# Performance work log

Measured on AMD Instinct MI355X. Metric: run time of the kernel, lower is better.

## Reference

```python
import jax, jax.numpy as jnp
import numpy as np

N = 50000
E = 600000
IN_CH = 128
HID = 256
OUT_CH = 64
R = 8


def setup_inputs() -> dict:
    key = jax.random.key(0)
    ks = jax.random.split(key, 12)
    x = jax.random.normal(ks[0], (N, IN_CH), dtype=jnp.float32)
    edge_index = jax.random.randint(ks[1], (2, E), 0, N, dtype=jnp.int32)
    edge_type = jax.random.randint(ks[2], (E,), 0, R, dtype=jnp.int32)
    s1 = 1.0 / np.sqrt(IN_CH)
    s2 = 1.0 / np.sqrt(HID)
    W1 = jax.random.uniform(ks[3], (R, IN_CH, HID), jnp.float32, -s1, s1)
    root1 = jax.random.uniform(ks[4], (IN_CH, HID), jnp.float32, -s1, s1)
    b1 = jnp.zeros((HID,), jnp.float32)
    W2 = jax.random.uniform(ks[5], (R, HID, HID), jnp.float32, -s2, s2)
    root2 = jax.random.uniform(ks[6], (HID, HID), jnp.float32, -s2, s2)
    b2 = jnp.zeros((HID,), jnp.float32)
    lin_W = jax.random.uniform(ks[7], (HID, OUT_CH), jnp.float32, -s2, s2)
    lin_b = jnp.zeros((OUT_CH,), jnp.float32)
    return {
        "x": x, "edge_index": edge_index, "edge_type": edge_type,
        "W1": W1, "root1": root1, "b1": b1,
        "W2": W2, "root2": root2, "b2": b2,
        "lin_W": lin_W, "lin_b": lin_b,
    }


def rgcn_conv(x, src, dst, edge_type, W, root, b):
    # out_i = root x_i + b + sum_r mean_{j in N_r(i)} W_r x_j  (PyG RGCNConv, aggr='mean')
    num_rel = W.shape[0]
    n = x.shape[0]
    out = x @ root + b
    x_src = x[src]  # [E, d_in] gathered once, masked per relation
    for r in range(num_rel):
        mask = (edge_type == r)
        msg = jnp.where(mask[:, None], x_src, 0.0)
        agg = jax.ops.segment_sum(msg, dst, num_segments=n)          # [N, d_in]
        cnt = jax.ops.segment_sum(mask.astype(x.dtype), dst, num_segments=n)
        agg = agg / jnp.maximum(cnt, 1.0)[:, None]                    # mean per relation
        out = out + agg @ W[r]
    return out


def reference(x, edge_index, edge_type, W1, root1, b1, W2, root2, b2, lin_W, lin_b):
    src, dst = edge_index[0], edge_index[1]
    h = jax.nn.relu(rgcn_conv(x, src, dst, edge_type, W1, root1, b1))
    h = jax.nn.relu(rgcn_conv(h, src, dst, edge_type, W2, root2, b2))
    logits = h @ lin_W + lin_b
    return jax.nn.log_softmax(logits, axis=-1)
```

## Files before the change

### kernel.cpp

```cpp
#include <hip/hip_runtime.h>
#include <hip/hip_bf16.h>

#define N_NODES 50000
#define E_EDGES 600000
#define IN_CH 128
#define HID 256
#define OUT_CH 64
#define NREL 8
#define HALF1 25000

typedef __attribute__((ext_vector_type(8))) short bf16x8;
typedef __attribute__((ext_vector_type(4))) float f32x4;

__device__ __forceinline__ float bf2f(unsigned short u) {
    union { unsigned int i; float f; } x; x.i = ((unsigned int)u) << 16; return x.f;
}
__device__ __forceinline__ unsigned short f2bf(float f) {
    __hip_bfloat16 b = __float2bfloat16(f);
    return *reinterpret_cast<unsigned short*>(&b);
}
__device__ __forceinline__ void gload_lds16(const void* g, void* l) {
    __builtin_amdgcn_global_load_lds(
        (const __attribute__((address_space(1))) unsigned int*)g,
        (__attribute__((address_space(3))) unsigned int*)l, 16, 0, 0);
}

__global__ void k_deg(const int* __restrict__ dst, int* __restrict__ deg) {
    int e = blockIdx.x * blockDim.x + threadIdx.x;
    if (e < E_EDGES) atomicAdd(&deg[dst[e]], 1);
}

__global__ __launch_bounds__(256) void k_scanA(const int* __restrict__ deg,
                                               int* __restrict__ offs,
                                               int* __restrict__ bsum) {
    __shared__ int wexcl[4];
    const int tid = threadIdx.x;
    const int lane = tid & 63;
    const int wid = tid >> 6;
    const int i = blockIdx.x * 256 + tid;
    const int v = (i < N_NODES) ? deg[i] : 0;
    int incl = v;
#pragma unroll
    for (int s = 1; s < 64; s <<= 1) {
        int t = __shfl_up(incl, s);
        if (lane >= s) incl += t;
    }
    __shared__ int wsum[4];
    if (lane == 63) wsum[wid] = incl;
    __syncthreads();
    if (tid == 0) {
        int run = 0;
#pragma unroll
        for (int w = 0; w < 4; w++) { wexcl[w] = run; run += wsum[w]; }
        bsum[blockIdx.x] = run;
    }
    __syncthreads();
    if (i < N_NODES) offs[i] = wexcl[wid] + incl - v;
}

__global__ __launch_bounds__(256) void k_scanB(int* __restrict__ bsum, int nb) {
    __shared__ int wexcl[4];
    __shared__ int wsum[4];
    const int tid = threadIdx.x;
    const int lane = tid & 63;
    const int wid = tid >> 6;
    const int v = (tid < nb) ? bsum[tid] : 0;
    int incl = v;
#pragma unroll
    for (int s = 1; s < 64; s <<= 1) {
        int t = __shfl_up(incl, s);
        if (lane >= s) incl += t;
    }
    if (lane == 63) wsum[wid] = incl;
    __syncthreads();
    if (tid == 0) {
        int run = 0;
#pragma unroll
        for (int w = 0; w < 4; w++) { wexcl[w] = run; run += wsum[w]; }
    }
    __syncthreads();
    if (tid < nb) bsum[tid] = wexcl[wid] + incl - v;
}

__global__ __launch_bounds__(256) void k_scanC(int* __restrict__ offs,
                                               const int* __restrict__ bsum) {
    const int i = blockIdx.x * 256 + threadIdx.x;
    if (i < N_NODES) offs[i] += bsum[blockIdx.x];
    if (i == 0) offs[N_NODES] = E_EDGES;
}

__global__ void k_place(const int* __restrict__ src, const int* __restrict__ dst,
                        const int* __restrict__ etype, const int* __restrict__ offs,
                        int* __restrict__ cursor, int* __restrict__ ekey) {
    int e = blockIdx.x * blockDim.x + threadIdx.x;
    if (e < E_EDGES) {
        int d = dst[e];
        int p = atomicAdd(&cursor[d], 1);
        ekey[offs[d] + p] = (etype[e] << 16) | src[e];
    }
}

__global__ __launch_bounds__(256) void k_wsort(const int* __restrict__ offs,
                                               int* __restrict__ ekey,
                                               int* __restrict__ relOffs) {
    const int w = threadIdx.x >> 6;
    const int t = threadIdx.x & 63;
    const int i = blockIdx.x * 4 + w;
    if (i >= N_NODES) return;
    const int lo = offs[i], hi = offs[i + 1];
    const int deg = hi - lo;
    if (deg == 0) {
        if (t < 9) relOffs[i * 9 + t] = lo;
        return;
    }
    if (deg <= 64) {
        const int key = (t < deg) ? ekey[lo + t] : 0x7FFFFFFF;
        int rank = 0;
#pragma unroll
        for (int s = 0; s < 64; s++) {
            const int ok = __shfl(key, s);
            rank += (int)((ok < key) | ((ok == key) & (s < t)));
        }
        if (t < deg) ekey[lo + rank] = key;
        const int rel = key >> 16;
        if (t == 0) relOffs[i * 9] = lo;
        int run = lo;
#pragma unroll
        for (int r = 0; r < NREL; r++) {
            unsigned long long b = __ballot((t < deg) && (rel == r));
            run += (int)__popcll(b);
            if (t == 0) relOffs[i * 9 + r + 1] = run;
        }
    } else if (t == 0) {
        for (int a = lo + 1; a < hi; a++) {
            int k = ekey[a];
            int b = a - 1;
            while (b >= lo && ekey[b] > k) { ekey[b + 1] = ekey[b]; b--; }
            ekey[b + 1] = k;
        }
        int p = lo;
        relOffs[i * 9] = lo;
#pragma unroll
        for (int r = 0; r < NREL; r++) {
            while (p < hi && (ekey[p] >> 16) == r) p++;
            relOffs[i * 9 + r + 1] = p;
        }
    }
}

#define PREP_CVT 6250
#define PREP_WT1 1152
#define PREP_WT2 2304
#define PREP_WT3 128
__global__ __launch_bounds__(256) void k_prep(const float* __restrict__ x,
                                              unsigned short* __restrict__ xb,
                                              const float* __restrict__ root1,
                                              const float* __restrict__ W1,
                                              unsigned short* __restrict__ Wt1,
                                              const float* __restrict__ root2,
                                              const float* __restrict__ W2,
                                              unsigned short* __restrict__ Wt2,
                                              const float* __restrict__ linW,
                                              unsigned short* __restrict__ linWt) {
    const int b = blockIdx.x;
    if (b < PREP_CVT) {
        int i = b * 256 + threadIdx.x;
        float4 v = *(const float4*)&x[i * 4];
        short4 o;
        o.x = (short)f2bf(v.x); o.y = (short)f2bf(v.y);
        o.z = (short)f2bf(v.z); o.w = (short)f2bf(v.w);
        *(short4*)&xb[i * 4] = o;
    } else if (b < PREP_CVT + PREP_WT1) {
        int idx = (b - PREP_CVT) * 256 + threadIdx.x;
        int c = idx / 1152, k = idx % 1152;
        float v = (k < IN_CH) ? root1[k * 256 + c] : W1[(size_t)(k - IN_CH) * 256 + c];
        Wt1[idx] = f2bf(v);
    } else if (b < PREP_CVT + PREP_WT1 + PREP_WT2) {
        int idx = (b - PREP_CVT - PREP_WT1) * 256 + threadIdx.x;
        int c = idx / 2304, k = idx % 2304;
        float v = (k < HID) ? root2[k * 256 + c] : W2[(size_t)(k - HID) * 256 + c];
        Wt2[idx] = f2bf(v);
    } else {
        int idx = (b - PREP_CVT - PREP_WT1 - PREP_WT2) * 256 + threadIdx.x;
        int rp = idx / 256, k = idx % 256;
        int c = rp & 63;
        float w = linW[k * OUT_CH + c];
        unsigned short hi = f2bf(w);
        linWt[idx] = (rp < 64) ? hi : f2bf(w - bf2f(hi));
    }
}

template <int CH>
__global__ __launch_bounds__(256) void k_agg8(const unsigned short* __restrict__ xin,
                                              const int* __restrict__ relOffs,
                                              const int* __restrict__ ekey,
                                              unsigned short* __restrict__ agg,
                                              int base, int count) {
    const int w = threadIdx.x >> 6;
    const int t = threadIdx.x & 63;
    const int rel_node = blockIdx.x * 4 + w;
    if (rel_node >= count) return;
    const int node = base + rel_node;
    constexpr int VPT = CH / 64;
    const unsigned short* xcol = xin + t * VPT;
    unsigned short* orow = agg + (size_t)rel_node * (NREL * CH) + t * VPT;
    const int* ro = relOffs + node * 9;
    const int lo = ro[0];
    const int deg = ro[8] - lo;

    if (deg == 0) {
#pragma unroll
        for (int r = 0; r < NREL; r++) {
            if (VPT == 4) *(short4*)(orow + r * CH) = make_short4(0, 0, 0, 0);
            else *(short2*)(orow + r * CH) = make_short2(0, 0);
        }
        return;
    }

    if (deg <= 64) {
        const int kv = ekey[lo + ((t < deg) ? t : 0)];
#pragma unroll
        for (int r = 0; r < NREL; r++) {
            const int s = ro[r] - lo, e = ro[r + 1] - lo;
            const int len = e - s;
            float a0 = 0.f, a1 = 0.f, a2 = 0.f, a3 = 0.f;
            int j = s;
            for (; j + 2 <= e; j += 2) {
                const int k0 = __shfl(kv, j) & 0xFFFF;
                const int k1 = __shfl(kv, j + 1) & 0xFFFF;
                if (VPT == 4) {
                    short4 v0 = *(const short4*)(xcol + (size_t)k0 * CH);
                    short4 v1 = *(const short4*)(xcol + (size_t)k1 * CH);
                    a0 += bf2f((unsigned short)v0.x);
                    a1 += bf2f((unsigned short)v0.y);
                    a2 += bf2f((unsigned short)v0.z);
                    a3 += bf2f((unsigned short)v0.w);
                    a0 += bf2f((unsigned short)v1.x);
                    a1 += bf2f((unsigned short)v1.y);
                    a2 += bf2f((unsigned short)v1.z);
                    a3 += bf2f((unsigned short)v1.w);
                } else {
                    short2 v0 = *(const short2*)(xcol + (size_t)k0 * CH);
                    short2 v1 = *(const short2*)(xcol + (size_t)k1 * CH);
                    a0 += bf2f((unsigned short)v0.x);
                    a1 += bf2f((unsigned short)v0.y);
                    a0 += bf2f((unsigned short)v1.x);
                    a1 += bf2f((unsigned short)v1.y);
                }
            }
            if (j < e) {
                const int k0 = __shfl(kv, j) & 0xFFFF;
                if (VPT == 4) {
                    short4 v0 = *(const short4*)(xcol + (size_t)k0 * CH);
                    a0 += bf2f((unsigned short)v0.x);
                    a1 += bf2f((unsigned short)v0.y);
                    a2 += bf2f((unsigned short)v0.z);
                    a3 += bf2f((unsigned short)v0.w);
                } else {
                    short2 v0 = *(const short2*)(xcol + (size_t)k0 * CH);
                    a0 += bf2f((unsigned short)v0.x);
                    a1 += bf2f((unsigned short)v0.y);
                }
            }
            const float inv = (len > 0) ? 1.0f / (float)len : 0.0f;
            if (VPT == 4) {
                short4 o;
                o.x = (short)f2bf(a0 * inv);
                o.y = (short)f2bf(a1 * inv);
                o.z = (short)f2bf(a2 * inv);
                o.w = (short)f2bf(a3 * inv);
                *(short4*)(orow + r * CH) = o;
            } else {
                short2 o;
                o.x = (short)f2bf(a0 * inv);
                o.y = (short)f2bf(a1 * inv);
                *(short2*)(orow + r * CH) = o;
            }
        }
    } else {
#pragma unroll
        for (int r = 0; r < NREL; r++) {
            const int s = ro[r], e = ro[r + 1];
            float a0 = 0.f, a1 = 0.f, a2 = 0.f, a3 = 0.f;
            for (int ee = s; ee < e; ee++) {
                const int k = ekey[ee] & 0xFFFF;
                if (VPT == 4) {
                    short4 v = *(const short4*)(xcol + (size_t)k * CH);
                    a0 += bf2f((unsigned short)v.x);
                    a1 += bf2f((unsigned short)v.y);
                    a2 += bf2f((unsigned short)v.z);
                    a3 += bf2f((unsigned short)v.w);
                } else {
                    short2 v = *(const short2*)(xcol + (size_t)k * CH);
                    a0 += bf2f((unsigned short)v.x);
                    a1 += bf2f((unsigned short)v.y);
                }
            }
            const float inv = (e > s) ? 1.0f / (float)(e - s) : 0.0f;
            if (VPT == 4) {
                short4 o;
                o.x = (short)f2bf(a0 * inv);
                o.y = (short)f2bf(a1 * inv);
                o.z = (short)f2bf(a2 * inv);
                o.w = (short)f2bf(a3 * inv);
                *(short4*)(orow + r * CH) = o;
            } else {
                short2 o;
                o.x = (short)f2bf(a0 * inv);
                o.y = (short)f2bf(a1 * inv);
                *(short2*)(orow + r * CH) = o;
            }
        }
    }
}

__global__ __launch_bounds__(256) void k_mgemm(
    const unsigned short* __restrict__ Aroot, int rootK, int ldroot,
    const unsigned short* __restrict__ Aagg, int ldagg,
    const unsigned short* __restrict__ Wt, int ldWt, int Ktot,
    const float* __restrict__ bias, unsigned short* __restrict__ hbOut, int M,
    int rowsPerXcd) {
    __shared__ __align__(16) unsigned short Al[2][128 * 64];
    __shared__ __align__(16) unsigned short Bl[2][128 * 64];
    const int p = blockIdx.x;
    const int xcd = p & 7;
    const int col = (p >> 3) & 1;
    const int rIdx = p >> 4;
    const int row = xcd * rowsPerXcd + rIdx;
    if (row * 128 >= M) return;
    const int bm = row * 128;
    const int bn = col * 128;
    const int tid = threadIdx.x;
    const int wv = tid >> 6, ln = tid & 63;
    const int wr = (wv & 1) * 64;
    const int wc = (wv >> 1) * 64;
    const int lg = ln >> 4;
    const int lr = ln & 15;

    f32x4 acc[4][4];
#pragma unroll
    for (int m = 0; m < 4; m++)
#pragma unroll
        for (int n = 0; n < 4; n++) acc[m][n] = (f32x4){0.f, 0.f, 0.f, 0.f};

    int baseR[4], baseG[4], baseB[4];
#pragma unroll
    for (int q = 0; q < 4; q++) {
        int t = (wv * 4 + q) * 64 + ln;
        int r = t >> 3, ps = t & 7;
        int slog = ps ^ (r & 7);
        int rg = bm + r; if (rg > M - 1) rg = M - 1;
        baseR[q] = (rootK > 0) ? (rg * ldroot + slog * 8) : 0;
        baseG[q] = rg * ldagg + slog * 8 - rootK;
        baseB[q] = (bn + r) * ldWt + slog * 8;
    }

    auto stage = [&](int k0, int buf) {
        const bool inRoot = (k0 < rootK);
#pragma unroll
        for (int q = 0; q < 4; q++) {
            const unsigned short* sa =
                inRoot ? (Aroot + baseR[q] + k0) : (Aagg + baseG[q] + k0);
            gload_lds16(sa, &Al[buf][(wv * 4 + q) * 512]);
        }
#pragma unroll
        for (int q = 0; q < 4; q++) {
            gload_lds16(Wt + baseB[q] + k0, &Bl[buf][(wv * 4 + q) * 512]);
        }
    };

    const int nt = Ktot >> 6;
    stage(0, 0);
    asm volatile("s_waitcnt vmcnt(0)" ::: "memory");
    __syncthreads();

    int cur = 0;
    for (int t = 0; t < nt; ++t) {
        if (t + 1 < nt) stage((t + 1) << 6, cur ^ 1);
        __builtin_amdgcn_s_setprio(1);
#pragma unroll
        for (int kk = 0; kk < 2; kk++) {
            bf16x8 af[4], bfr[4];
#pragma unroll
            for (int m = 0; m < 4; m++) {
                int r = wr + 16 * m + lr;
                int ph = (kk * 4 + lg) ^ (r & 7);
                af[m] = *(const bf16x8*)&Al[cur][r * 64 + ph * 8];
            }
#pragma unroll
            for (int n = 0; n < 4; n++) {
                int c = wc + 16 * n + lr;
                int ph = (kk * 4 + lg) ^ (c & 7);
                bfr[n] = *(const bf16x8*)&Bl[cur][c * 64 + ph * 8];
            }
#pragma unroll
            for (int m = 0; m < 4; m++)
#pragma unroll
                for (int n = 0; n < 4; n++)
                    acc[m][n] = __builtin_amdgcn_mfma_f32_16x16x32_bf16(
                        af[m], bfr[n], acc[m][n], 0, 0, 0);
        }
        __builtin_amdgcn_s_setprio(0);
        if (t + 1 < nt) {
            asm volatile("s_waitcnt vmcnt(0)" ::: "memory");
            __syncthreads();
            cur ^= 1;
        }
    }

#pragma unroll
    for (int m = 0; m < 4; m++) {
#pragma unroll
        for (int reg = 0; reg < 4; reg++) {
            int r = bm + wr + 16 * m + lg * 4 + reg;
            if (r >= M) continue;
#pragma unroll
            for (int n = 0; n < 4; n++) {
                int c = bn + wc + 16 * n + lr;
                float v = acc[m][n][reg] + bias[c];
                hbOut[(size_t)r * 256 + c] = f2bf(fmaxf(v, 0.f));
            }
        }
    }
}

__global__ __launch_bounds__(256) void k_final3(const unsigned short* __restrict__ h,
                                                const unsigned short* __restrict__ linWt,
                                                const float* __restrict__ bias,
                                                float* __restrict__ out, int M) {
    __shared__ __align__(16) unsigned short Al[128 * 64];
    __shared__ __align__(16) unsigned short Bl[128 * 64];
    const int bm = blockIdx.x * 128;
    const int tid = threadIdx.x;
    const int wv = tid >> 6, ln = tid & 63;
    const int wr = wv * 32;
    const int lg = ln >> 4;
    const int lr = ln & 15;

    f32x4 acc[2][8];
#pragma unroll
    for (int m = 0; m < 2; m++)
#pragma unroll
        for (int n = 0; n < 8; n++) acc[m][n] = (f32x4){0.f, 0.f, 0.f, 0.f};

    int baseA[4], baseB[4];
#pragma unroll
    for (int q = 0; q < 4; q++) {
        int t = (wv * 4 + q) * 64 + ln;
        int r = t >> 3, ps = t & 7;
        int slog = ps ^ (r & 7);
        int rg = bm + r; if (rg > M - 1) rg = M - 1;
        baseA[q] = rg * HID + slog * 8;
        baseB[q] = r * HID + slog * 8;
    }

    for (int t = 0; t < 4; ++t) {
        if (t > 0) __syncthreads();
        const int k0 = t << 6;
#pragma unroll
        for (int q = 0; q < 4; q++)
            gload_lds16(h + baseA[q] + k0, &Al[(wv * 4 + q) * 512]);
#pragma unroll
        for (int q = 0; q < 4; q++)
            gload_lds16(linWt + baseB[q] + k0, &Bl[(wv * 4 + q) * 512]);
        asm volatile("s_waitcnt vmcnt(0)" ::: "memory");
        __syncthreads();
#pragma unroll
        for (int kk = 0; kk < 2; kk++) {
            bf16x8 af[2], bfr[8];
#pragma unroll
            for (int m = 0; m < 2; m++) {
                int r = wr + 16 * m + lr;
                int ph = (kk * 4 + lg) ^ (r & 7);
                af[m] = *(const bf16x8*)&Al[r * 64 + ph * 8];
            }
#pragma unroll
            for (int n = 0; n < 8; n++) {
                int c = n * 16 + lr;
                int ph = (kk * 4 + lg) ^ (c & 7);
                bfr[n] = *(const bf16x8*)&Bl[c * 64 + ph * 8];
            }
#pragma unroll
            for (int m = 0; m < 2; m++)
#pragma unroll
                for (int n = 0; n < 8; n++)
                    acc[m][n] = __builtin_amdgcn_mfma_f32_16x16x32_bf16(
                        af[m], bfr[n], acc[m][n], 0, 0, 0);
        }
    }

    float b4[4];
#pragma unroll
    for (int n = 0; n < 4; n++) b4[n] = bias[n * 16 + lr];
#pragma unroll
    for (int m = 0; m < 2; m++) {
#pragma unroll
        for (int reg = 0; reg < 4; reg++) {
            const int row = bm + wr + 16 * m + lg * 4 + reg;
            float v0 = acc[m][0][reg] + acc[m][4][reg] + b4[0];
            float v1 = acc[m][1][reg] + acc[m][5][reg] + b4[1];
            float v2 = acc[m][2][reg] + acc[m][6][reg] + b4[2];
            float v3 = acc[m][3][reg] + acc[m][7][reg] + b4[3];
            float mx = fmaxf(fmaxf(v0, v1), fmaxf(v2, v3));
#pragma unroll
            for (int s = 1; s < 16; s <<= 1) mx = fmaxf(mx, __shfl_xor(mx, s));
            float sum = expf(v0 - mx) + expf(v1 - mx) + expf(v2 - mx) + expf(v3 - mx);
#pragma unroll
            for (int s = 1; s < 16; s <<= 1) sum += __shfl_xor(sum, s);
            const float lse = mx + logf(sum);
            if (row < M) {
                float* orow = out + (size_t)row * OUT_CH + lr;
                orow[0]  = v0 - lse;
                orow[16] = v1 - lse;
                orow[32] = v2 - lse;
                orow[48] = v3 - lse;
            }
        }
    }
}

extern "C" void kernel_launch(void* const* d_in, const int* in_sizes, int n_in,
                              void* d_out, int out_size, void* d_ws, size_t ws_size,
                              hipStream_t stream) {
    const float* x     = (const float*)d_in[0];
    const int*   eidx  = (const int*)d_in[1];
    const int*   etype = (const int*)d_in[2];
    const float* W1    = (const float*)d_in[3];
    const float* root1 = (const float*)d_in[4];
    const float* b1    = (const float*)d_in[5];
    const float* W2    = (const float*)d_in[6];
    const float* root2 = (const float*)d_in[7];
    const float* b2    = (const float*)d_in[8];
    const float* linW  = (const float*)d_in[9];
    const float* linb  = (const float*)d_in[10];
    float* out = (float*)d_out;
    const int* srcI = eidx;
    const int* dstI = eidx + E_EDGES;

    char* ws = (char*)d_ws;
    size_t off = 0;
    auto alloc = [&](size_t bytes) {
        size_t o = off;
        off += (bytes + 255) & ~(size_t)255;
        return ws + o;
    };
    unsigned short* xb    = (unsigned short*)alloc((size_t)N_NODES * IN_CH * 2);
    unsigned short* hb1   = (unsigned short*)alloc((size_t)N_NODES * HID * 2);
    unsigned short* hb2   = (unsigned short*)alloc((size_t)N_NODES * HID * 2);
    unsigned short* Wt1   = (unsigned short*)alloc((size_t)256 * 1152 * 2);
    unsigned short* Wt2   = (unsigned short*)alloc((size_t)256 * 2304 * 2);
    unsigned short* linWt = (unsigned short*)alloc((size_t)128 * 256 * 2);
    int* deg     = (int*)alloc((size_t)N_NODES * 4);
    int* cursor  = (int*)alloc((size_t)N_NODES * 4);
    int* offs    = (int*)alloc((size_t)(N_NODES + 1) * 4);
    int* ekey    = (int*)alloc((size_t)E_EDGES * 4);
    int* relOffs = (int*)alloc((size_t)N_NODES * 9 * 4);
    int* bsum    = (int*)alloc((size_t)256 * 4);
    unsigned short* agg = (unsigned short*)(ws + off);
    const size_t avail = (ws_size > off) ? ws_size - off : 0;
    const bool l2single = avail >= (size_t)N_NODES * NREL * HID * 2;

    k_prep<<<PREP_CVT + PREP_WT1 + PREP_WT2 + PREP_WT3, 256, 0, stream>>>(
        x, xb, root1, W1, Wt1, root2, W2, Wt2, linW, linWt);
    hipMemsetAsync(deg, 0, (size_t)N_NODES * 4, stream);
    hipMemsetAsync(cursor, 0, (size_t)N_NODES * 4, stream);
    k_deg<<<(E_EDGES + 255) / 256, 256, 0, stream>>>(dstI, deg);
    const int nb = (N_NODES + 255) / 256;
    k_scanA<<<nb, 256, 0, stream>>>(deg, offs, bsum);
    k_scanB<<<1, 256, 0, stream>>>(bsum, nb);
    k_scanC<<<nb, 256, 0, stream>>>(offs, bsum);
    k_place<<<(E_EDGES + 255) / 256, 256, 0, stream>>>(srcI, dstI, etype, offs, cursor, ekey);
    k_wsort<<<(N_NODES + 3) / 4, 256, 0, stream>>>(offs, ekey, relOffs);

    auto mkGrid = [](int M, int& rpx) {
        int nRow = (M + 127) / 128;
        rpx = (nRow + 7) / 8;
        return 16 * rpx;
    };

    {
        int rpx;
        const int nG = mkGrid(N_NODES, rpx);
        k_agg8<IN_CH><<<(N_NODES + 3) / 4, 256, 0, stream>>>(xb, relOffs, ekey, agg,
                                                             0, N_NODES);
        k_mgemm<<<nG, 256, 0, stream>>>(xb, IN_CH, IN_CH, agg, NREL * IN_CH,
                                        Wt1, 1152, 1152, b1, hb1, N_NODES, rpx);
    }

    if (l2single) {
        int rpx;
        const int nG = mkGrid(N_NODES, rpx);
        k_agg8<HID><<<(N_NODES + 3) / 4, 256, 0, stream>>>(hb1, relOffs, ekey, agg,
                                                           0, N_NODES);
        k_mgemm<<<nG, 256, 0, stream>>>(hb1, HID, HID, agg, NREL * HID,
                                        Wt2, 2304, 2304, b2, hb2, N_NODES, rpx);
    } else {
        for (int c = 0; c < 2; c++) {
            const int base = c * HALF1;
            int rpx;
            const int nG = mkGrid(HALF1, rpx);
            k_agg8<HID><<<(HALF1 + 3) / 4, 256, 0, stream>>>(hb1, relOffs, ekey, agg,
                                                             base, HALF1);
            k_mgemm<<<nG, 256, 0, stream>>>(hb1 + (size_t)base * HID, HID, HID,
                                            agg, NREL * HID, Wt2, 2304, 2304, b2,
                                            hb2 + (size_t)base * HID, HALF1, rpx);
        }
    }

    k_final3<<<(N_NODES + 127) / 128, 256, 0, stream>>>(hb2, linWt, linb, out, N_NODES);
}
```

Measured before the change: 402.8 us.

## Fuse per-relation mean aggregation into the RGCN GEMM A-tile loading

Drops the separate aggregation kernel and its large bf16 intermediate buffer. The GEMM now builds each aggregated A tile itself, by gathering neighbour features per relation straight into shared memory, and streams only the root part and the weights from global memory. This avoids writing and re-reading the aggregation buffer, including the split-in-halves path. In exchange, the gathers are repeated for each output-column tile. They are also scalar, latency-bound loads done inside the GEMM loop with no overlap, and the A tile loses its double buffering.

Result: slower. 1.587 ms (+293.9%).

```diff
diff --git a/kernel.cpp b/kernel.cpp
--- a/kernel.cpp
+++ b/kernel.cpp
@@ -7,7 +7,6 @@
 #define HID 256
 #define OUT_CH 64
 #define NREL 8
-#define HALF1 25000
 
 typedef __attribute__((ext_vector_type(8))) short bf16x8;
 typedef __attribute__((ext_vector_type(4))) float f32x4;
@@ -191,137 +190,15 @@
 }
 
 template <int CH>
-__global__ __launch_bounds__(256) void k_agg8(const unsigned short* __restrict__ xin,
-                                              const int* __restrict__ relOffs,
-                                              const int* __restrict__ ekey,
-                                              unsigned short* __restrict__ agg,
-                                              int base, int count) {
-    const int w = threadIdx.x >> 6;
-    const int t = threadIdx.x & 63;
-    const int rel_node = blockIdx.x * 4 + w;
-    if (rel_node >= count) return;
-    const int node = base + rel_node;
-    constexpr int VPT = CH / 64;
-    const unsigned short* xcol = xin + t * VPT;
-    unsigned short* orow = agg + (size_t)rel_node * (NREL * CH) + t * VPT;
-    const int* ro = relOffs + node * 9;
-    const int lo = ro[0];
-    const int deg = ro[8] - lo;
-
-    if (deg == 0) {
-#pragma unroll
-        for (int r = 0; r < NREL; r++) {
-            if (VPT == 4) *(short4*)(orow + r * CH) = make_short4(0, 0, 0, 0);
-            else *(short2*)(orow + r * CH) = make_short2(0, 0);
-        }
-        return;
-    }
-
-    if (deg <= 64) {
-        const int kv = ekey[lo + ((t < deg) ? t : 0)];
-#pragma unroll
-        for (int r = 0; r < NREL; r++) {
-            const int s = ro[r] - lo, e = ro[r + 1] - lo;
-            const int len = e - s;
-            float a0 = 0.f, a1 = 0.f, a2 = 0.f, a3 = 0.f;
-            int j = s;
-            for (; j + 2 <= e; j += 2) {
-                const int k0 = __shfl(kv, j) & 0xFFFF;
-                const int k1 = __shfl(kv, j + 1) & 0xFFFF;
-                if (VPT == 4) {
-                    short4 v0 = *(const short4*)(xcol + (size_t)k0 * CH);
-                    short4 v1 = *(const short4*)(xcol + (size_t)k1 * CH);
-                    a0 += bf2f((unsigned short)v0.x);
-                    a1 += bf2f((unsigned short)v0.y);
-                    a2 += bf2f((unsigned short)v0.z);
-                    a3 += bf2f((unsigned short)v0.w);
-                    a0 += bf2f((unsigned short)v1.x);
-                    a1 += bf2f((unsigned short)v1.y);
-                    a2 += bf2f((unsigned short)v1.z);
-                    a3 += bf2f((unsigned short)v1.w);
-                } else {
-                    short2 v0 = *(const short2*)(xcol + (size_t)k0 * CH);
-                    short2 v1 = *(const short2*)(xcol + (size_t)k1 * CH);
-                    a0 += bf2f((unsigned short)v0.x);
-                    a1 += bf2f((unsigned short)v0.y);
-                    a0 += bf2f((unsigned short)v1.x);
-                    a1 += bf2f((unsigned short)v1.y);
-                }
-            }
-            if (j < e) {
-                const int k0 = __shfl(kv, j) & 0xFFFF;
-                if (VPT == 4) {
-                    short4 v0 = *(const short4*)(xcol + (size_t)k0 * CH);
-                    a0 += bf2f((unsigned short)v0.x);
-                    a1 += bf2f((unsigned short)v0.y);
-                    a2 += bf2f((unsigned short)v0.z);
-                    a3 += bf2f((unsigned short)v0.w);
-                } else {
-                    short2 v0 = *(const short2*)(xcol + (size_t)k0 * CH);
-                    a0 += bf2f((unsigned short)v0.x);
-                    a1 += bf2f((unsigned short)v0.y);
-                }
-            }
-            const float inv = (len > 0) ? 1.0f / (float)len : 0.0f;
-            if (VPT == 4) {
-                short4 o;
-                o.x = (short)f2bf(a0 * inv);
-                o.y = (short)f2bf(a1 * inv);
-                o.z = (short)f2bf(a2 * inv);
-                o.w = (short)f2bf(a3 * inv);
-                *(short4*)(orow + r * CH) = o;
-            } else {
-                short2 o;
-                o.x = (short)f2bf(a0 * inv);
-                o.y = (short)f2bf(a1 * inv);
-                *(short2*)(orow + r * CH) = o;
-            }
-        }
-    } else {
-#pragma unroll
-        for (int r = 0; r < NREL; r++) {
-            const int s = ro[r], e = ro[r + 1];
-            float a0 = 0.f, a1 = 0.f, a2 = 0.f, a3 = 0.f;
-            for (int ee = s; ee < e; ee++) {
-                const int k = ekey[ee] & 0xFFFF;
-                if (VPT == 4) {
-                    short4 v = *(const short4*)(xcol + (size_t)k * CH);
-                    a0 += bf2f((unsigned short)v.x);
-                    a1 += bf2f((unsigned short)v.y);
-                    a2 += bf2f((unsigned short)v.z);
-                    a3 += bf2f((unsigned short)v.w);
-                } else {
-                    short2 v = *(const short2*)(xcol + (size_t)k * CH);
-                    a0 += bf2f((unsigned short)v.x);
-                    a1 += bf2f((unsigned short)v.y);
-                }
-            }
-            const float inv = (e > s) ? 1.0f / (float)(e - s) : 0.0f;
-            if (VPT == 4) {
-                short4 o;
-                o.x = (short)f2bf(a0 * inv);
-                o.y = (short)f2bf(a1 * inv);
-                o.z = (short)f2bf(a2 * inv);
-                o.w = (short)f2bf(a3 * inv);
-                *(short4*)(orow + r * CH) = o;
-            } else {
-                short2 o;
-                o.x = (short)f2bf(a0 * inv);
-                o.y = (short)f2bf(a1 * inv);
-                *(short2*)(orow + r * CH) = o;
-            }
-        }
-    }
-}
-
-__global__ __launch_bounds__(256) void k_mgemm(
-    const unsigned short* __restrict__ Aroot, int rootK, int ldroot,
-    const unsigned short* __restrict__ Aagg, int ldagg,
+__global__ __launch_bounds__(256) void k_fgemm(
+    const unsigned short* __restrict__ Aroot,
     const unsigned short* __restrict__ Wt, int ldWt, int Ktot,
+    const int* __restrict__ relOffs, const int* __restrict__ ekey,
     const float* __restrict__ bias, unsigned short* __restrict__ hbOut, int M,
     int rowsPerXcd) {
-    __shared__ __align__(16) unsigned short Al[2][128 * 64];
+    __shared__ __align__(16) unsigned short Al[128 * 64];
     __shared__ __align__(16) unsigned short Bl[2][128 * 64];
+    const int rootK = CH;
     const int p = blockIdx.x;
     const int xcd = p & 7;
     const int col = (p >> 3) & 1;
@@ -343,40 +220,86 @@
 #pragma unroll
         for (int n = 0; n < 4; n++) acc[m][n] = (f32x4){0.f, 0.f, 0.f, 0.f};
 
-    int baseR[4], baseG[4], baseB[4];
+    int baseR[4], baseB[4];
 #pragma unroll
     for (int q = 0; q < 4; q++) {
         int t = (wv * 4 + q) * 64 + ln;
         int r = t >> 3, ps = t & 7;
         int slog = ps ^ (r & 7);
         int rg = bm + r; if (rg > M - 1) rg = M - 1;
-        baseR[q] = (rootK > 0) ? (rg * ldroot + slog * 8) : 0;
-        baseG[q] = rg * ldagg + slog * 8 - rootK;
+        baseR[q] = rg * CH + slog * 8;
         baseB[q] = (bn + r) * ldWt + slog * 8;
     }
 
-    auto stage = [&](int k0, int buf) {
-        const bool inRoot = (k0 < rootK);
-#pragma unroll
-        for (int q = 0; q < 4; q++) {
-            const unsigned short* sa =
-                inRoot ? (Aroot + baseR[q] + k0) : (Aagg + baseG[q] + k0);
-            gload_lds16(sa, &Al[buf][(wv * 4 + q) * 512]);
-        }
-#pragma unroll
-        for (int q = 0; q < 4; q++) {
+    auto stageB = [&](int k0, int buf) {
+#pragma unroll
+        for (int q = 0; q < 4; q++)
             gload_lds16(Wt + baseB[q] + k0, &Bl[buf][(wv * 4 + q) * 512]);
-        }
     };
+    auto stageAroot = [&](int k0) {
+#pragma unroll
+        for (int q = 0; q < 4; q++)
+            gload_lds16(Aroot + baseR[q] + k0, &Al[(wv * 4 + q) * 512]);
+    };
 
     const int nt = Ktot >> 6;
-    stage(0, 0);
-    asm volatile("s_waitcnt vmcnt(0)" ::: "memory");
-    __syncthreads();
-
+    stageB(0, 0);
     int cur = 0;
+
     for (int t = 0; t < nt; ++t) {
-        if (t + 1 < nt) stage((t + 1) << 6, cur ^ 1);
+        const int k0 = t << 6;
+        if (t + 1 < nt) stageB((t + 1) << 6, cur ^ 1);
+
+        if (k0 < rootK) {
+            stageAroot(k0);
+        } else {
+            const int ka = k0 - rootK;
+            const int rel = ka / CH;
+            const int c0 = ka & (CH - 1);
+            const unsigned short* srcF = Aroot + c0 + ln;
+            const int r0 = wv * 32;
+#pragma unroll
+            for (int g = 0; g < 4; g++) {
+                int sA[8], eA[8];
+                float ac[8];
+#pragma unroll
+                for (int rr = 0; rr < 8; rr++) {
+                    int node = bm + r0 + g * 8 + rr;
+                    if (node > M - 1) node = M - 1;
+                    sA[rr] = relOffs[node * 9 + rel];
+                    eA[rr] = relOffs[node * 9 + rel + 1];
+                    ac[rr] = 0.f;
+                }
+                int mx = 0;
+#pragma unroll
+                for (int rr = 0; rr < 8; rr++) {
+                    int l = eA[rr] - sA[rr];
+                    if (l > mx) mx = l;
+                }
+                for (int q = 0; q < mx; q++) {
+#pragma unroll
+                    for (int rr = 0; rr < 8; rr++) {
+                        int jj = sA[rr] + q;
+                        int lim = eA[rr] - 1;
+                        if (lim < 0) lim = 0;
+                        if (jj > lim) jj = lim;
+                        const int key = ekey[jj] & 0xFFFF;
+                        const float v = bf2f(srcF[(size_t)key * CH]);
+                        ac[rr] += (sA[rr] + q < eA[rr]) ? v : 0.f;
+                    }
+                }
+#pragma unroll
+                for (int rr = 0; rr < 8; rr++) {
+                    const int len = eA[rr] - sA[rr];
+                    const float inv = (len > 0) ? 1.0f / (float)len : 0.0f;
+                    const int ii = r0 + g * 8 + rr;
+                    Al[ii * 64 + (((ln >> 3) ^ (ii & 7)) << 3) + (ln & 7)] =
+                        f2bf(ac[rr] * inv);
+                }
+            }
+        }
+
+        __syncthreads();
         __builtin_amdgcn_s_setprio(1);
 #pragma unroll
         for (int kk = 0; kk < 2; kk++) {
@@ -385,7 +308,7 @@
             for (int m = 0; m < 4; m++) {
                 int r = wr + 16 * m + lr;
                 int ph = (kk * 4 + lg) ^ (r & 7);
-                af[m] = *(const bf16x8*)&Al[cur][r * 64 + ph * 8];
+                af[m] = *(const bf16x8*)&Al[r * 64 + ph * 8];
             }
 #pragma unroll
             for (int n = 0; n < 4; n++) {
@@ -401,11 +324,8 @@
                         af[m], bfr[n], acc[m][n], 0, 0, 0);
         }
         __builtin_amdgcn_s_setprio(0);
-        if (t + 1 < nt) {
-            asm volatile("s_waitcnt vmcnt(0)" ::: "memory");
-            __syncthreads();
-            cur ^= 1;
-        }
+        __syncthreads();
+        cur ^= 1;
     }
 
 #pragma unroll
@@ -556,9 +476,6 @@
     int* ekey    = (int*)alloc((size_t)E_EDGES * 4);
     int* relOffs = (int*)alloc((size_t)N_NODES * 9 * 4);
     int* bsum    = (int*)alloc((size_t)256 * 4);
-    unsigned short* agg = (unsigned short*)(ws + off);
-    const size_t avail = (ws_size > off) ? ws_size - off : 0;
-    const bool l2single = avail >= (size_t)N_NODES * NREL * HID * 2;
 
     k_prep<<<PREP_CVT + PREP_WT1 + PREP_WT2 + PREP_WT3, 256, 0, stream>>>(
         x, xb, root1, W1, Wt1, root2, W2, Wt2, linW, linWt);
@@ -578,34 +495,14 @@
         return 16 * rpx;
     };
 
-    {
-        int rpx;
-        const int nG = mkGrid(N_NODES, rpx);
-        k_agg8<IN_CH><<<(N_NODES + 3) / 4, 256, 0, stream>>>(xb, relOffs, ekey, agg,
-                                                             0, N_NODES);
-        k_mgemm<<<nG, 256, 0, stream>>>(xb, IN_CH, IN_CH, agg, NREL * IN_CH,
-                                        Wt1, 1152, 1152, b1, hb1, N_NODES, rpx);
-    }
-
-    if (l2single) {
-        int rpx;
-        const int nG = mkGrid(N_NODES, rpx);
-        k_agg8<HID><<<(N_NODES + 3) / 4, 256, 0, stream>>>(hb1, relOffs, ekey, agg,
-                                                           0, N_NODES);
-        k_mgemm<<<nG, 256, 0, stream>>>(hb1, HID, HID, agg, NREL * HID,
-                                        Wt2, 2304, 2304, b2, hb2, N_NODES, rpx);
-    } else {
-        for (int c = 0; c < 2; c++) {
-            const int base = c * HALF1;
-            int rpx;
-            const int nG = mkGrid(HALF1, rpx);
-            k_agg8<HID><<<(HALF1 + 3) / 4, 256, 0, stream>>>(hb1, relOffs, ekey, agg,
-                                                             base, HALF1);
-            k_mgemm<<<nG, 256, 0, stream>>>(hb1 + (size_t)base * HID, HID, HID,
-                                            agg, NREL * HID, Wt2, 2304, 2304, b2,
-                                            hb2 + (size_t)base * HID, HALF1, rpx);
-        }
-    }
+    int rpx;
+    const int nG = mkGrid(N_NODES, rpx);
+
+    k_fgemm<IN_CH><<<nG, 256, 0, stream>>>(xb, Wt1, 1152, 1152, relOffs, ekey,
+                                           b1, hb1, N_NODES, rpx);
+
+    k_fgemm<HID><<<nG, 256, 0, stream>>>(hb1, Wt2, 2304, 2304, relOffs, ekey,
+                                         b2, hb2, N_NODES, rpx);
 
     k_final3<<<(N_NODES + 127) / 128, 256, 0, stream>>>(hb2, linWt, linb, out, N_NODES);
 }
```
